# Performance work log

Measured on AMD Instinct MI355X. Metric: run time of the kernel, lower is better.

Reference implementation:

```python
import jax, jax.numpy as jnp
import numpy as np

NH, DH = 16, 64          # n_head, d_head
CH = NH + DH             # 80
RQ, RK, RV = 6, 2, 2
ROPE_BASE = 10000.0


def _rotary(b, cache_len):
    # b: [B, T, R, DH]; rotates the d-factor exactly as the torch Rotary module
    T = b.shape[1]
    inv_freq = (1.0 / ROPE_BASE) ** (jnp.arange(0, DH, 2, dtype=jnp.float32) / DH)
    t = jnp.arange(T, dtype=jnp.float32) + cache_len
    freqs = jnp.outer(t, inv_freq)                      # [T, DH/2]
    cos = freqs[None, :, None, :].astype(b.dtype)
    sin = jnp.sin(freqs)[None, :, None, :].astype(b.dtype)
    cos = jnp.cos(freqs)[None, :, None, :].astype(b.dtype)
    x1, x2 = jnp.split(b, 2, axis=3)
    return jnp.concatenate([x1 * cos + x2 * sin, -x1 * sin + x2 * cos], axis=3)


def setup_inputs() -> dict:
    key = jax.random.key(0)
    k1, k2, k3, k4 = jax.random.split(key, 4)
    B, T, D = 2, 2048, 1024
    x = jax.random.normal(k1, (B, T, D), dtype=jnp.float32)
    # xavier-uniform-like scale for factor projections
    s_q = float(np.sqrt(6.0 / (D + CH)))
    s_o = float(np.sqrt(6.0 / (D + D)))
    W_abq = jax.random.uniform(k2, (RQ * CH, D), minval=-s_q, maxval=s_q, dtype=jnp.float32)
    W_abkv = jax.random.uniform(k3, ((RK + RV) * CH, D), minval=-s_q, maxval=s_q, dtype=jnp.float32)
    W_o = jax.random.uniform(k4, (D, D), minval=-s_o, maxval=s_o, dtype=jnp.float32)
    return {"x": x, "W_abq": W_abq, "W_abkv": W_abkv, "W_o": W_o}


def reference(x, W_abq, W_abkv, W_o):
    B, T, D = x.shape
    # low-rank factor projections
    abq = (x @ W_abq.T).reshape(B, T, RQ, CH)
    a_q, b_q = abq[..., :NH], abq[..., NH:]            # [B,T,RQ,NH], [B,T,RQ,DH]
    abkv = (x @ W_abkv.T).reshape(B, T, RK + RV, CH)
    a_kv = abkv[..., :NH]
    b_kv = _rotary(abkv[..., NH:], cache_len=0)        # RoPE applied to K/V d-factors only
    a_k, b_k = a_kv[:, :, :RK], b_kv[:, :, :RK]
    a_v, b_v = a_kv[:, :, RK:], b_kv[:, :, RK:]
    # tensor-product reconstruction of Q/K/V
    q = jnp.einsum('btrh,btrd->bthd', a_q, b_q) / RQ
    k = jnp.einsum('btrh,btrd->bthd', a_k, b_k) / RK
    v = jnp.einsum('btrh,btrd->bthd', a_v, b_v) / RV
    # causal attention (flex_attention default scale = 1/sqrt(dh))
    scale = 1.0 / jnp.sqrt(jnp.asarray(DH, dtype=q.dtype))
    scores = jnp.einsum('bqhd,bkhd->bhqk', q, k) * scale
    causal = jnp.tril(jnp.ones((T, T), dtype=bool))
    scores = jnp.where(causal[None, None], scores, jnp.finfo(scores.dtype).min)
    attn = jax.nn.softmax(scores, axis=-1)
    y = jnp.einsum('bhqk,bkhd->bqhd', attn, v).reshape(B, T, D)
    return y @ W_o.T
```

## Files before the change

### kernel.cpp

```cpp
#include <hip/hip_runtime.h>
#include <hip/hip_bf16.h>
#include <math.h>

#define NHEADS 16
#define DHEAD  64
#define CHDIM  80
#define RQn    6
#define RKn    2
#define RVn    2
#define BB     2
#define TT     2048
#define DDim   1024
#define NQK    800

using frag16 = __attribute__((ext_vector_type(8))) short;
using f32x4  = __attribute__((ext_vector_type(4))) float;
using f32x16 = __attribute__((ext_vector_type(16))) float;

#define AS1(p) ((const __attribute__((address_space(1))) unsigned int*)(p))
#define AS3(p) ((__attribute__((address_space(3))) unsigned int*)(p))

static __device__ __forceinline__ unsigned short bf16_bits(float f) {
    __hip_bfloat16 h = __float2bfloat16(f);
    return *(unsigned short*)&h;
}
static __device__ __forceinline__ unsigned int pk2(float a, float b) {
    return ((unsigned int)bf16_bits(b) << 16) | (unsigned int)bf16_bits(a);
}

__global__ __launch_bounds__(256) void cvt_all(
    const float* __restrict__ x, const float* __restrict__ wq,
    const float* __restrict__ wk, const float* __restrict__ wo,
    __hip_bfloat16* __restrict__ xb, __hip_bfloat16* __restrict__ wqk,
    __hip_bfloat16* __restrict__ wob)
{
    int bid = blockIdx.x;
    const float* src; __hip_bfloat16* dst; int n4;
    if (bid < 4096)      { src = x;  dst = xb;            n4 = 1048576; }
    else if (bid < 4576) { bid -= 4096; src = wq; dst = wqk;           n4 = 122880; }
    else if (bid < 4896) { bid -= 4576; src = wk; dst = wqk + 491520;  n4 = 81920; }
    else                 { bid -= 4896; src = wo; dst = wob;           n4 = 262144; }
    int i = bid * 256 + threadIdx.x;
    if (i < n4) {
        float4 v = *(const float4*)&src[i * 4];
        ushort4 o;
        o.x = bf16_bits(v.x); o.y = bf16_bits(v.y);
        o.z = bf16_bits(v.z); o.w = bf16_bits(v.w);
        *(ushort4*)&dst[i * 4] = o;
    }
}

__global__ __launch_bounds__(256) void gemm_bf16(
    const __hip_bfloat16* __restrict__ A, const __hip_bfloat16* __restrict__ W,
    float* __restrict__ C, int M, int N, int K)
{
    __shared__ __hip_bfloat16 Asl[128 * 64];
    __shared__ __hip_bfloat16 Bsl[128 * 64];
    const int tid = threadIdx.x;
    const int w = tid >> 6, lane = tid & 63;
    const int l16 = lane & 15, quad = lane >> 4;
    const int wr = w >> 1, wc = w & 1;
    const int bm = blockIdx.y * 128, bn = blockIdx.x * 128;

    int rS[4], cS[4], rBS[4];
    #pragma unroll
    for (int j = 0; j < 4; j++) {
        int L = (w * 4 + j) * 64 + lane;
        rS[j] = L >> 3;
        cS[j] = (L & 7) ^ (rS[j] & 7);
        int rb = bn + rS[j];
        rBS[j] = (rb < N) ? rb : (N - 1);
    }

    f32x4 acc[4][4];
    #pragma unroll
    for (int mt = 0; mt < 4; mt++)
        #pragma unroll
        for (int nt = 0; nt < 4; nt++)
            acc[mt][nt] = (f32x4){0.f, 0.f, 0.f, 0.f};

    for (int k0 = 0; k0 < K; k0 += 64) {
        #pragma unroll
        for (int j = 0; j < 4; j++) {
            const __hip_bfloat16* ga = A + (size_t)(bm + rS[j]) * K + k0 + cS[j] * 8;
            const __hip_bfloat16* gb = W + (size_t)rBS[j] * K + k0 + cS[j] * 8;
            __builtin_amdgcn_global_load_lds(AS1(ga), AS3(&Asl[(w * 4 + j) * 512]), 16, 0, 0);
            __builtin_amdgcn_global_load_lds(AS1(gb), AS3(&Bsl[(w * 4 + j) * 512]), 16, 0, 0);
        }
        __syncthreads();
        #pragma unroll
        for (int ks = 0; ks < 2; ks++) {
            frag16 af[4], bf[4];
            #pragma unroll
            for (int mt = 0; mt < 4; mt++) {
                int r = wr * 64 + mt * 16 + l16;
                af[mt] = *(const frag16*)&Asl[r * 64 + (((ks * 4 + quad) ^ (r & 7)) * 8)];
            }
            #pragma unroll
            for (int nt = 0; nt < 4; nt++) {
                int r = wc * 64 + nt * 16 + l16;
                bf[nt] = *(const frag16*)&Bsl[r * 64 + (((ks * 4 + quad) ^ (r & 7)) * 8)];
            }
            #pragma unroll
            for (int mt = 0; mt < 4; mt++)
                #pragma unroll
                for (int nt = 0; nt < 4; nt++)
                    acc[mt][nt] = __builtin_amdgcn_mfma_f32_16x16x32_bf16(af[mt], bf[nt], acc[mt][nt], 0, 0, 0);
        }
        __syncthreads();
    }
    #pragma unroll
    for (int mt = 0; mt < 4; mt++) {
        #pragma unroll
        for (int reg = 0; reg < 4; reg++) {
            int row = bm + wr * 64 + mt * 16 + quad * 4 + reg;
            #pragma unroll
            for (int nt = 0; nt < 4; nt++) {
                int col = bn + wc * 64 + nt * 16 + l16;
                if (col < N) C[(size_t)row * N + col] = acc[mt][nt][reg];
            }
        }
    }
}

__global__ __launch_bounds__(256) void qkv_kernel(
    const float* __restrict__ ab,
    __hip_bfloat16* __restrict__ q, __hip_bfloat16* __restrict__ k,
    __hip_bfloat16* __restrict__ vT)
{
    const int tok0 = blockIdx.x * 4;
    const int w = threadIdx.x >> 6;
    const int d = threadIdx.x & 63;
    const int token = tok0 + w;
    const int b = token / TT;
    const int t = token % TT;
    __shared__ float sq[4][RQn * CHDIM];
    __shared__ float skv[4][(RKn + RVn) * CHDIM];
    __shared__ __align__(8) __hip_bfloat16 vbuf[NHEADS][DHEAD][4];
    const float* aq  = ab + (size_t)token * NQK;
    const float* akv = aq + 480;
    for (int i = d; i < RQn * CHDIM; i += 64) sq[w][i] = aq[i];
    for (int i = d; i < (RKn + RVn) * CHDIM; i += 64) skv[w][i] = akv[i];
    const int i32 = d & 31;
    float inv_freq = powf(10000.0f, -(float)i32 / 32.0f);
    float fr = (float)t * inv_freq;
    float c = cosf(fr), s = sinf(fr);
    float rot[4];
    #pragma unroll
    for (int r = 0; r < 4; r++) {
        float x1 = skv[w][r * CHDIM + NHEADS + i32];
        float x2 = skv[w][r * CHDIM + NHEADS + 32 + i32];
        rot[r] = (d < 32) ? (x1 * c + x2 * s) : (-x1 * s + x2 * c);
    }
    float bqv[RQn];
    #pragma unroll
    for (int r = 0; r < RQn; r++) bqv[r] = sq[w][r * CHDIM + NHEADS + d];
    #pragma unroll
    for (int h = 0; h < NHEADS; h++) {
        float accq = 0.0f;
        #pragma unroll
        for (int r = 0; r < RQn; r++)
            accq += sq[w][r * CHDIM + h] * bqv[r];
        q[((size_t)(b * NHEADS + h) * TT + t) * DHEAD + d] = __float2bfloat16(accq * (0.125f / 6.0f));
        float acck = 0.0f, accv = 0.0f;
        #pragma unroll
        for (int r = 0; r < RKn; r++)
            acck += skv[w][r * CHDIM + h] * rot[r];
        #pragma unroll
        for (int r = 0; r < RVn; r++)
            accv += skv[w][(RKn + r) * CHDIM + h] * rot[RKn + r];
        k[((size_t)(b * NHEADS + h) * TT + t) * DHEAD + d] = __float2bfloat16(acck * 0.5f);
        vbuf[h][d][w] = __float2bfloat16(accv * 0.5f);
    }
    __syncthreads();
    const int t0 = tok0 % TT;
    const int b0 = tok0 / TT;
    for (int row = threadIdx.x; row < NHEADS * DHEAD; row += 256) {
        int h = row >> 6, dd = row & 63;
        *(uint2*)&vT[((size_t)(b0 * NHEADS + h) * DHEAD + dd) * TT + t0] =
            *(const uint2*)&vbuf[h][dd][0];
    }
}

__global__ __launch_bounds__(256, 3) void flash_mfma(
    const __hip_bfloat16* __restrict__ q, const __hip_bfloat16* __restrict__ k,
    const __hip_bfloat16* __restrict__ vT, __hip_bfloat16* __restrict__ y)
{
    const int L = blockIdx.x;
    const int bh = L & 31;
    const int rr = L >> 5;
    const int qt = (L < 256) ? rr : (15 - (rr & 7));
    const int b = bh >> 4, h = bh & 15;
    const int tid = threadIdx.x;
    const int w = tid >> 6;
    const int lane = tid & 63;
    const int l31 = lane & 31;
    const int hi = lane >> 5;
    const int xi = l31 & 7;
    const int paddr = (lane ^ 32) << 2;

    __shared__ __align__(16) __hip_bfloat16 KsF[4096];
    __shared__ __align__(16) __hip_bfloat16 VsF[4096];

    const size_t base = (size_t)bh * TT * DHEAD;
    const __hip_bfloat16* qb = q + base;
    const __hip_bfloat16* kb = k + base;
    const __hip_bfloat16* vb = vT + base;

    const int qrow0 = qt * 128 + w * 32;
    const int qlane = qrow0 + l31;
    const int ktd = qrow0 >> 6;

    int offK[2], offV[2];
    #pragma unroll
    for (int j = 0; j < 2; j++) {
        int Lc = w * 128 + j * 64 + lane;
        int r = Lc >> 3, c8 = Lc & 7, g8 = c8 ^ (r & 7);
        offK[j] = r * 64 + g8 * 8;
        offV[j] = r * TT + g8 * 8;
    }

    frag16 qB[4];
    #pragma unroll
    for (int kt4 = 0; kt4 < 4; kt4++)
        qB[kt4] = *(const frag16*)&qb[(size_t)qlane * DHEAD + kt4 * 16 + hi * 8];

    f32x16 O0 = {}, O1 = {};
    float lpart = 0.0f;

    const int nkt = 2 * qt + 2;
    for (int kt = 0; kt < nkt; kt++) {
        #pragma unroll
        for (int j = 0; j < 2; j++) {
            __builtin_amdgcn_global_load_lds(AS1(kb + (size_t)kt * 4096 + offK[j]),
                                             AS3(&KsF[w * 1024 + j * 512]), 16, 0, 0);
            __builtin_amdgcn_global_load_lds(AS1(vb + (size_t)kt * 64 + offV[j]),
                                             AS3(&VsF[w * 1024 + j * 512]), 16, 0, 0);
        }
        __syncthreads();

        if (kt <= ktd) {
            f32x16 ST0 = {}, ST1 = {};
            #pragma unroll
            for (int kt4 = 0; kt4 < 4; kt4++) {
                int c8 = kt4 * 2 + hi;
                frag16 kf0 = *(const frag16*)&KsF[l31 * 64 + ((c8 ^ xi) * 8)];
                frag16 kf1 = *(const frag16*)&KsF[(32 + l31) * 64 + ((c8 ^ xi) * 8)];
                ST0 = __builtin_amdgcn_mfma_f32_32x32x16_bf16(kf0, qB[kt4], ST0, 0, 0, 0);
                ST1 = __builtin_amdgcn_mfma_f32_32x32x16_bf16(kf1, qB[kt4], ST1, 0, 0, 0);
            }
            float* s0 = (float*)&ST0;
            float* s1 = (float*)&ST1;
            if (kt == ktd) {
                int kb0 = kt * 64 + 4 * hi;
                #pragma unroll
                for (int reg = 0; reg < 16; reg++) {
                    int rowc = (reg & 3) + 8 * (reg >> 2);
                    if (kb0 + rowc > qlane)      s0[reg] = -1e30f;
                    if (kb0 + 32 + rowc > qlane) s1[reg] = -1e30f;
                }
            }
            #pragma unroll
            for (int reg = 0; reg < 16; reg++) {
                float p0 = __expf(s0[reg]);
                float p1 = __expf(s1[reg]);
                s0[reg] = p0; s1[reg] = p1;
                lpart += p0 + p1;
            }
            frag16 Pf[4];
            #pragma unroll
            for (int k2 = 0; k2 < 4; k2++) {
                const float* sF = (k2 >= 2) ? s1 : s0;
                const int bs = 8 * (k2 & 1);
                unsigned int u0a = pk2(sF[bs + 0], sF[bs + 1]);
                unsigned int u0b = pk2(sF[bs + 2], sF[bs + 3]);
                unsigned int u1a = pk2(sF[bs + 4], sF[bs + 5]);
                unsigned int u1b = pk2(sF[bs + 6], sF[bs + 7]);
                unsigned int r0a = (unsigned int)__builtin_amdgcn_ds_bpermute(paddr, (int)u0a);
                unsigned int r0b = (unsigned int)__builtin_amdgcn_ds_bpermute(paddr, (int)u0b);
                unsigned int r1a = (unsigned int)__builtin_amdgcn_ds_bpermute(paddr, (int)u1a);
                unsigned int r1b = (unsigned int)__builtin_amdgcn_ds_bpermute(paddr, (int)u1b);
                union { frag16 f; unsigned int u[4]; } pf;
                pf.u[0] = hi ? r1a : u0a;
                pf.u[1] = hi ? r1b : u0b;
                pf.u[2] = hi ? u1a : r0a;
                pf.u[3] = hi ? u1b : r0b;
                Pf[k2] = pf.f;
            }
            #pragma unroll
            for (int k2 = 0; k2 < 4; k2++) {
                int c8 = k2 * 2 + hi;
                frag16 vf0 = *(const frag16*)&VsF[l31 * 64 + ((c8 ^ xi) * 8)];
                frag16 vf1 = *(const frag16*)&VsF[(32 + l31) * 64 + ((c8 ^ xi) * 8)];
                O0 = __builtin_amdgcn_mfma_f32_32x32x16_bf16(vf0, Pf[k2], O0, 0, 0, 0);
                O1 = __builtin_amdgcn_mfma_f32_32x32x16_bf16(vf1, Pf[k2], O1, 0, 0, 0);
            }
        }
        __syncthreads();
    }

    float lother = __int_as_float(__builtin_amdgcn_ds_bpermute(paddr, __float_as_int(lpart)));
    float inv = 1.0f / (lpart + lother);
    float* o0 = (float*)&O0;
    float* o1 = (float*)&O1;
    __hip_bfloat16* yp = y + ((size_t)(b * TT + qlane)) * DDim + h * DHEAD;
    #pragma unroll
    for (int g = 0; g < 4; g++) {
        int d0 = 8 * g + 4 * hi;
        uint2 pa, pb;
        pa.x = pk2(o0[4*g+0] * inv, o0[4*g+1] * inv);
        pa.y = pk2(o0[4*g+2] * inv, o0[4*g+3] * inv);
        pb.x = pk2(o1[4*g+0] * inv, o1[4*g+1] * inv);
        pb.y = pk2(o1[4*g+2] * inv, o1[4*g+3] * inv);
        *(uint2*)&yp[d0] = pa;
        *(uint2*)&yp[32 + d0] = pb;
    }
}

extern "C" void kernel_launch(void* const* d_in, const int* in_sizes, int n_in,
                              void* d_out, int out_size, void* d_ws, size_t ws_size,
                              hipStream_t stream) {
    const float* x      = (const float*)d_in[0];
    const float* W_abq  = (const float*)d_in[1];
    const float* W_abkv = (const float*)d_in[2];
    const float* W_o    = (const float*)d_in[3];
    float* out = (float*)d_out;

    char* ws = (char*)d_ws;
    __hip_bfloat16* xb   = (__hip_bfloat16*)ws;  ws += (size_t)4194304 * 2;
    __hip_bfloat16* wqk  = (__hip_bfloat16*)ws;  ws += (size_t)NQK * 1024 * 2;
    __hip_bfloat16* wo_b = (__hip_bfloat16*)ws;  ws += (size_t)1048576 * 2;
    float* abqkv = (float*)ws;                   ws += (size_t)4096 * NQK * 4;
    __hip_bfloat16* qb = (__hip_bfloat16*)ws;    ws += (size_t)4194304 * 2;
    __hip_bfloat16* kb = (__hip_bfloat16*)ws;    ws += (size_t)4194304 * 2;
    __hip_bfloat16* vT = (__hip_bfloat16*)ws;    ws += (size_t)4194304 * 2;
    __hip_bfloat16* yb = (__hip_bfloat16*)ws;    ws += (size_t)4194304 * 2;

    cvt_all<<<dim3(5920), dim3(256), 0, stream>>>(x, W_abq, W_abkv, W_o, xb, wqk, wo_b);
    gemm_bf16<<<dim3(7, 32), dim3(256), 0, stream>>>(xb, wqk, abqkv, 4096, NQK, 1024);
    qkv_kernel<<<dim3(1024), dim3(256), 0, stream>>>(abqkv, qb, kb, vT);
    flash_mfma<<<dim3(512), dim3(256), 0, stream>>>(qb, kb, vT, yb);
    gemm_bf16<<<dim3(8, 32), dim3(256), 0, stream>>>(yb, wo_b, out, 4096, 1024, 1024);
}
```

Before: 188.2 us.

## Double-buffer LDS tiles in GEMM and flash attention to prefetch next tile

Both the bf16 GEMM and the flash-attention kernel now keep two LDS buffers. The global-to-LDS loads for the next K tile, or the next K/V tile, are issued right after the barrier, while the current tile is consumed. This drops one barrier per iteration and aims to hide global memory latency behind the MFMA work. In exchange, LDS use per block doubles, which may lower occupancy in the GEMM. The compiler may also insert conservative vmcnt waits before the LDS reads, which could remove the overlap.

```diff
diff --git a/kernel.cpp b/kernel.cpp
--- a/kernel.cpp
+++ b/kernel.cpp
@@ -54,8 +54,8 @@
     const __hip_bfloat16* __restrict__ A, const __hip_bfloat16* __restrict__ W,
     float* __restrict__ C, int M, int N, int K)
 {
-    __shared__ __hip_bfloat16 Asl[128 * 64];
-    __shared__ __hip_bfloat16 Bsl[128 * 64];
+    __shared__ __hip_bfloat16 Asl[2][128 * 64];
+    __shared__ __hip_bfloat16 Bsl[2][128 * 64];
     const int tid = threadIdx.x;
     const int w = tid >> 6, lane = tid & 63;
     const int l16 = lane & 15, quad = lane >> 4;
@@ -79,27 +79,40 @@
         for (int nt = 0; nt < 4; nt++)
             acc[mt][nt] = (f32x4){0.f, 0.f, 0.f, 0.f};
 
-    for (int k0 = 0; k0 < K; k0 += 64) {
-        #pragma unroll
-        for (int j = 0; j < 4; j++) {
-            const __hip_bfloat16* ga = A + (size_t)(bm + rS[j]) * K + k0 + cS[j] * 8;
-            const __hip_bfloat16* gb = W + (size_t)rBS[j] * K + k0 + cS[j] * 8;
-            __builtin_amdgcn_global_load_lds(AS1(ga), AS3(&Asl[(w * 4 + j) * 512]), 16, 0, 0);
-            __builtin_amdgcn_global_load_lds(AS1(gb), AS3(&Bsl[(w * 4 + j) * 512]), 16, 0, 0);
-        }
+    const int nK = K >> 6;
+    #pragma unroll
+    for (int j = 0; j < 4; j++) {
+        const __hip_bfloat16* ga = A + (size_t)(bm + rS[j]) * K + cS[j] * 8;
+        const __hip_bfloat16* gb = W + (size_t)rBS[j] * K + cS[j] * 8;
+        __builtin_amdgcn_global_load_lds(AS1(ga), AS3(&Asl[0][(w * 4 + j) * 512]), 16, 0, 0);
+        __builtin_amdgcn_global_load_lds(AS1(gb), AS3(&Bsl[0][(w * 4 + j) * 512]), 16, 0, 0);
+    }
+
+    for (int kk = 0; kk < nK; kk++) {
+        const int cur = kk & 1;
         __syncthreads();
+        if (kk + 1 < nK) {
+            const int k1 = (kk + 1) * 64;
+            #pragma unroll
+            for (int j = 0; j < 4; j++) {
+                const __hip_bfloat16* ga = A + (size_t)(bm + rS[j]) * K + k1 + cS[j] * 8;
+                const __hip_bfloat16* gb = W + (size_t)rBS[j] * K + k1 + cS[j] * 8;
+                __builtin_amdgcn_global_load_lds(AS1(ga), AS3(&Asl[cur ^ 1][(w * 4 + j) * 512]), 16, 0, 0);
+                __builtin_amdgcn_global_load_lds(AS1(gb), AS3(&Bsl[cur ^ 1][(w * 4 + j) * 512]), 16, 0, 0);
+            }
+        }
         #pragma unroll
         for (int ks = 0; ks < 2; ks++) {
             frag16 af[4], bf[4];
             #pragma unroll
             for (int mt = 0; mt < 4; mt++) {
                 int r = wr * 64 + mt * 16 + l16;
-                af[mt] = *(const frag16*)&Asl[r * 64 + (((ks * 4 + quad) ^ (r & 7)) * 8)];
+                af[mt] = *(const frag16*)&Asl[cur][r * 64 + (((ks * 4 + quad) ^ (r & 7)) * 8)];
             }
             #pragma unroll
             for (int nt = 0; nt < 4; nt++) {
                 int r = wc * 64 + nt * 16 + l16;
-                bf[nt] = *(const frag16*)&Bsl[r * 64 + (((ks * 4 + quad) ^ (r & 7)) * 8)];
+                bf[nt] = *(const frag16*)&Bsl[cur][r * 64 + (((ks * 4 + quad) ^ (r & 7)) * 8)];
             }
             #pragma unroll
             for (int mt = 0; mt < 4; mt++)
@@ -107,7 +120,6 @@
                 for (int nt = 0; nt < 4; nt++)
                     acc[mt][nt] = __builtin_amdgcn_mfma_f32_16x16x32_bf16(af[mt], bf[nt], acc[mt][nt], 0, 0, 0);
         }
-        __syncthreads();
     }
     #pragma unroll
     for (int mt = 0; mt < 4; mt++) {
@@ -199,8 +211,8 @@
     const int xi = l31 & 7;
     const int paddr = (lane ^ 32) << 2;
 
-    __shared__ __align__(16) __hip_bfloat16 KsF[4096];
-    __shared__ __align__(16) __hip_bfloat16 VsF[4096];
+    __shared__ __align__(16) __hip_bfloat16 KsF[2][4096];
+    __shared__ __align__(16) __hip_bfloat16 VsF[2][4096];
 
     const size_t base = (size_t)bh * TT * DHEAD;
     const __hip_bfloat16* qb = q + base;
@@ -229,23 +241,35 @@
     float lpart = 0.0f;
 
     const int nkt = 2 * qt + 2;
+    #pragma unroll
+    for (int j = 0; j < 2; j++) {
+        __builtin_amdgcn_global_load_lds(AS1(kb + offK[j]),
+                                         AS3(&KsF[0][w * 1024 + j * 512]), 16, 0, 0);
+        __builtin_amdgcn_global_load_lds(AS1(vb + offV[j]),
+                                         AS3(&VsF[0][w * 1024 + j * 512]), 16, 0, 0);
+    }
+
     for (int kt = 0; kt < nkt; kt++) {
-        #pragma unroll
-        for (int j = 0; j < 2; j++) {
-            __builtin_amdgcn_global_load_lds(AS1(kb + (size_t)kt * 4096 + offK[j]),
-                                             AS3(&KsF[w * 1024 + j * 512]), 16, 0, 0);
-            __builtin_amdgcn_global_load_lds(AS1(vb + (size_t)kt * 64 + offV[j]),
-                                             AS3(&VsF[w * 1024 + j * 512]), 16, 0, 0);
-        }
+        const int cur = kt & 1;
         __syncthreads();
-
+        if (kt + 1 < nkt) {
+            #pragma unroll
+            for (int j = 0; j < 2; j++) {
+                __builtin_amdgcn_global_load_lds(AS1(kb + (size_t)(kt + 1) * 4096 + offK[j]),
+                                                 AS3(&KsF[cur ^ 1][w * 1024 + j * 512]), 16, 0, 0);
+                __builtin_amdgcn_global_load_lds(AS1(vb + (size_t)(kt + 1) * 64 + offV[j]),
+                                                 AS3(&VsF[cur ^ 1][w * 1024 + j * 512]), 16, 0, 0);
+            }
+        }
         if (kt <= ktd) {
+            const __hip_bfloat16* Kc = KsF[cur];
+            const __hip_bfloat16* Vc = VsF[cur];
             f32x16 ST0 = {}, ST1 = {};
             #pragma unroll
             for (int kt4 = 0; kt4 < 4; kt4++) {
                 int c8 = kt4 * 2 + hi;
-                frag16 kf0 = *(const frag16*)&KsF[l31 * 64 + ((c8 ^ xi) * 8)];
-                frag16 kf1 = *(const frag16*)&KsF[(32 + l31) * 64 + ((c8 ^ xi) * 8)];
+                frag16 kf0 = *(const frag16*)&Kc[l31 * 64 + ((c8 ^ xi) * 8)];
+                frag16 kf1 = *(const frag16*)&Kc[(32 + l31) * 64 + ((c8 ^ xi) * 8)];
                 ST0 = __builtin_amdgcn_mfma_f32_32x32x16_bf16(kf0, qB[kt4], ST0, 0, 0, 0);
                 ST1 = __builtin_amdgcn_mfma_f32_32x32x16_bf16(kf1, qB[kt4], ST1, 0, 0, 0);
             }
@@ -290,13 +314,12 @@
             #pragma unroll
             for (int k2 = 0; k2 < 4; k2++) {
                 int c8 = k2 * 2 + hi;
-                frag16 vf0 = *(const frag16*)&VsF[l31 * 64 + ((c8 ^ xi) * 8)];
-                frag16 vf1 = *(const frag16*)&VsF[(32 + l31) * 64 + ((c8 ^ xi) * 8)];
+                frag16 vf0 = *(const frag16*)&Vc[l31 * 64 + ((c8 ^ xi) * 8)];
+                frag16 vf1 = *(const frag16*)&Vc[(32 + l31) * 64 + ((c8 ^ xi) * 8)];
                 O0 = __builtin_amdgcn_mfma_f32_32x32x16_bf16(vf0, Pf[k2], O0, 0, 0, 0);
                 O1 = __builtin_amdgcn_mfma_f32_32x32x16_bf16(vf1, Pf[k2], O1, 0, 0, 0);
             }
         }
-        __syncthreads();
     }
 
     float lother = __int_as_float(__builtin_amdgcn_ds_bpermute(paddr, __float_as_int(lpart)));
```

After: 186.7 us. Within noise of the previous version (-0.8%).
